# Kernel tuning notes

Hardware: AMD Instinct MI355X
Metric: run time of the kernel (lower is better)

Reference implementation:

```python
import jax, jax.numpy as jnp
import numpy as np
import math

EMB = 512

def setup_inputs() -> dict:
    key = jax.random.key(0)
    ks = jax.random.split(key, 7)
    B, L, E = 4, 4096, EMB
    s = 1.0 / math.sqrt(E)
    return {
        "x": jax.random.normal(ks[0], (B, L, E), dtype=jnp.float32),
        "Wq": jax.random.normal(ks[1], (E, E), dtype=jnp.float32) * s,
        "bq": jax.random.normal(ks[2], (E,), dtype=jnp.float32) * 0.01,
        "Wk": jax.random.normal(ks[3], (E, E), dtype=jnp.float32) * s,
        "bk": jax.random.normal(ks[4], (E,), dtype=jnp.float32) * 0.01,
        "Wv": jax.random.normal(ks[5], (E, E), dtype=jnp.float32) * s,
        "bv": jax.random.normal(ks[6], (E,), dtype=jnp.float32) * 0.01,
    }

def reference(x, Wq, bq, Wk, bk, Wv, bv):
    # x: [B, L, E]; Linear weights stored torch-style [out, in]
    E = x.shape[-1]
    L = x.shape[1]
    q = jnp.einsum('ble,fe->blf', x, Wq) + bq
    k = jnp.einsum('ble,fe->blf', x, Wk) + bk
    v = jnp.einsum('ble,fe->blf', x, Wv) + bv
    qk = jnp.einsum('bqe,bke->bqk', q, k)  # [B, L, L]
    # causal mask: strict upper triangle filled with -1e9 BEFORE scaling (as in source)
    mask = jnp.triu(jnp.ones((L, L), dtype=bool), k=1)
    qk = jnp.where(mask, jnp.float32(-1e9), qk)
    att = jax.nn.softmax(qk / jnp.sqrt(jnp.float32(E)), axis=-1)
    return jnp.einsum('bqk,bke->bqe', att, v)
```

## Files before the change

kernel.cpp:

```cpp
#include <hip/hip_runtime.h>

typedef unsigned short u16;
typedef unsigned int u32;
typedef short bf16x8 __attribute__((ext_vector_type(8)));
typedef float f32x4 __attribute__((ext_vector_type(4)));
typedef u16 u16x8 __attribute__((ext_vector_type(8)));
typedef u16 u16x4 __attribute__((ext_vector_type(4)));

typedef const __attribute__((address_space(1))) u32* gas_ptr;
typedef __attribute__((address_space(3))) u32* las_ptr;

#define LQ   4096
#define EMB  512
#define NB   4
#define MROWS (NB * LQ)
#define QSCALE 0.04419417382415922f

__device__ __forceinline__ u16 f2bf(float f) {
  unsigned u = __builtin_bit_cast(unsigned, f);
  u += 0x7fffu + ((u >> 16) & 1u);
  return (u16)(u >> 16);
}
__device__ __forceinline__ float bf2f(u16 h) {
  unsigned u = ((unsigned)h) << 16;
  return __builtin_bit_cast(float, u);
}

__global__ void prep_w(const float* __restrict__ Wq, const float* __restrict__ bq,
                       const float* __restrict__ Wk, const float* __restrict__ bk,
                       const float* __restrict__ Wv, const float* __restrict__ bv,
                       u16* __restrict__ wqb, u16* __restrict__ wkb, u16* __restrict__ wvb,
                       float* __restrict__ bias) {
  int i = blockIdx.x * 256 + threadIdx.x;
  if (i < EMB * EMB) {
    wqb[i] = f2bf(Wq[i] * QSCALE);
    wkb[i] = f2bf(Wk[i]);
    wvb[i] = f2bf(Wv[i]);
  }
  if (i < EMB) {
    bias[i]           = bq[i] * QSCALE;
    bias[EMB + i]     = bk[i];
    bias[2 * EMB + i] = bv[i];
  }
}

__global__ void prep_x(const float* __restrict__ x, u16* __restrict__ xb) {
  int i = blockIdx.x * 256 + threadIdx.x;
  const float4* p = (const float4*)(x + (size_t)i * 8);
  float4 a = p[0], b = p[1];
  u16x8 o;
  o[0] = f2bf(a.x); o[1] = f2bf(a.y); o[2] = f2bf(a.z); o[3] = f2bf(a.w);
  o[4] = f2bf(b.x); o[5] = f2bf(b.y); o[6] = f2bf(b.z); o[7] = f2bf(b.w);
  *(u16x8*)(xb + (size_t)i * 8) = o;
}

__device__ __forceinline__ void stage128_256t(const u16* g, int ld, u16* lds, int tid) {
  int wave = tid >> 6;
#pragma unroll
  for (int p = 0; p < 4; ++p) {
    int c = tid + p * 256;
    int row = c >> 3, hh = c & 7;
    int h = hh ^ (row & 7);
    const u16* src = g + (size_t)row * ld + h * 8;
    u16* dst = lds + wave * 512 + p * 2048;
    __builtin_amdgcn_global_load_lds((gas_ptr)(const void*)src, (las_ptr)(void*)dst, 16, 0, 0);
  }
}

__device__ __forceinline__ void gemm_core_db(
    const u16* __restrict__ A, int lda,
    const u16* __restrict__ B, int ldb,
    int kIters, u16* lds,
    f32x4 acc[4][4], int tid, int lane, int wr, int wc)
{
  stage128_256t(A, lda, lds, tid);
  stage128_256t(B, ldb, lds + 8192, tid);
  for (int kb = 0; kb < kIters; ++kb) {
    u16* ldsA = lds + (kb & 1) * 16384;
    u16* ldsB = ldsA + 8192;
    __syncthreads();
    if (kb + 1 < kIters) {
      u16* nA = lds + ((kb + 1) & 1) * 16384;
      stage128_256t(A + (kb + 1) * 64, lda, nA, tid);
      stage128_256t(B + (kb + 1) * 64, ldb, nA + 8192, tid);
    }
#pragma unroll
    for (int s = 0; s < 2; ++s) {
      bf16x8 af[4], bfr[4];
#pragma unroll
      for (int m = 0; m < 4; ++m) {
        int row = wr * 64 + m * 16 + (lane & 15);
        int hh = (s * 4 + (lane >> 4)) ^ (row & 7);
        af[m] = *(const bf16x8*)(ldsA + row * 64 + hh * 8);
      }
#pragma unroll
      for (int n = 0; n < 4; ++n) {
        int row = wc * 64 + n * 16 + (lane & 15);
        int hh = (s * 4 + (lane >> 4)) ^ (row & 7);
        bfr[n] = *(const bf16x8*)(ldsB + row * 64 + hh * 8);
      }
#pragma unroll
      for (int m = 0; m < 4; ++m)
#pragma unroll
        for (int n = 0; n < 4; ++n)
          acc[m][n] = __builtin_amdgcn_mfma_f32_16x16x32_bf16(af[m], bfr[n], acc[m][n], 0, 0, 0);
    }
  }
}

__global__ __launch_bounds__(256, 2) void k_qkv(
    const u16* __restrict__ xb,
    const u16* __restrict__ w0, const u16* __restrict__ w1, const u16* __restrict__ w2,
    const float* __restrict__ bias,
    u16* __restrict__ o0, u16* __restrict__ o1, u16* __restrict__ o2)
{
  __shared__ __align__(16) u16 lds[32768];
  int bi = blockIdx.x;
  int which = bi >> 9;
  int t = bi & 511;
  int rt = t >> 2, ct = t & 3;
  const u16* W = (which == 0) ? w0 : (which == 1) ? w1 : w2;
  const float* bs = bias + which * EMB;
  int tid = threadIdx.x, lane = tid & 63, wave = tid >> 6;
  int wr = wave >> 1, wc = wave & 1;
  f32x4 acc[4][4];
#pragma unroll
  for (int m = 0; m < 4; ++m)
#pragma unroll
    for (int n = 0; n < 4; ++n) acc[m][n] = (f32x4)0.0f;

  gemm_core_db(xb + (size_t)rt * 128 * EMB, EMB,
               W + (size_t)ct * 128 * EMB, EMB, EMB / 64,
               lds, acc, tid, lane, wr, wc);

#pragma unroll
  for (int m = 0; m < 4; ++m)
#pragma unroll
    for (int n = 0; n < 4; ++n) {
      int row0 = rt * 128 + wr * 64 + m * 16 + ((lane >> 4) << 2);
      int col  = ct * 128 + wc * 64 + n * 16 + (lane & 15);
      float bv = bs[col];
      if (which < 2) {
        u16* out = (which == 0) ? o0 : o1;
#pragma unroll
        for (int r = 0; r < 4; ++r)
          out[(size_t)(row0 + r) * EMB + col] = f2bf(acc[m][n][r] + bv);
      } else {
        int b = row0 >> 12, l0 = row0 & (LQ - 1);
        u16x4 pk;
#pragma unroll
        for (int r = 0; r < 4; ++r) pk[r] = f2bf(acc[m][n][r] + bv);
        *(u16x4*)(o2 + ((size_t)(b * EMB + col)) * LQ + l0) = pk;
      }
    }
}

__global__ __launch_bounds__(256, 2) void k_qk(
    const u16* __restrict__ Q, const u16* __restrict__ K,
    u16* __restrict__ S, int bstart)
{
  __shared__ __align__(16) u16 lds[32768];
  int t = blockIdx.x;
  int b_local = t / 528;
  int i = t - b_local * 528;
  int qi = (int)((sqrtf(8.f * (float)i + 1.f) - 1.f) * 0.5f);
  while ((qi + 1) * (qi + 2) / 2 <= i) ++qi;
  while (qi * (qi + 1) / 2 > i) --qi;
  int ki = i - qi * (qi + 1) / 2;
  int bg = bstart + b_local;

  int tid = threadIdx.x, lane = tid & 63, wave = tid >> 6;
  int wr = wave >> 1, wc = wave & 1;
  f32x4 acc[4][4];
#pragma unroll
  for (int m = 0; m < 4; ++m)
#pragma unroll
    for (int n = 0; n < 4; ++n) acc[m][n] = (f32x4)0.0f;

  gemm_core_db(Q + ((size_t)bg * LQ + qi * 128) * EMB, EMB,
               K + ((size_t)bg * LQ + ki * 128) * EMB, EMB, EMB / 64,
               lds, acc, tid, lane, wr, wc);

  u16* Sb = S + (size_t)b_local * LQ * LQ;
#pragma unroll
  for (int m = 0; m < 4; ++m)
#pragma unroll
    for (int n = 0; n < 4; ++n) {
      int row0 = qi * 128 + wr * 64 + m * 16 + ((lane >> 4) << 2);
      int col  = ki * 128 + wc * 64 + n * 16 + (lane & 15);
#pragma unroll
      for (int r = 0; r < 4; ++r) {
        int row = row0 + r;
        float v = (col > row) ? -1e9f : acc[m][n][r];
        Sb[(size_t)row * LQ + col] = f2bf(v);
      }
    }
}

__global__ __launch_bounds__(1024, 4) void k_pv3(
    const u16* __restrict__ S, const u16* __restrict__ Vt,
    float* __restrict__ out, int bstart, int bcount)
{
  __shared__ __align__(16) u16 sV[32768];
  __shared__ __align__(16) u16 sP[8192];
  __shared__ float sF[128];
  __shared__ float sL[128];
  __shared__ int   sFlag[16];

  int bi = blockIdx.x;
  int per = 2 * bcount;
  int rt = bi / per;
  int rem = bi - rt * per;
  int ct = rem / bcount;
  int b_local = rem - ct * bcount;
  int bg = bstart + b_local;
  int units = 2 * (rt + 1);

  const u16* Sbase = S + ((size_t)b_local * LQ + rt * 128) * LQ;
  const u16* Vb = Vt + ((size_t)bg * EMB + ct * 256) * LQ;

  int tid = threadIdx.x, lane = tid & 63, wave = tid >> 6;
  int l15 = lane & 15, lhi = lane >> 4;
  int wr = wave >> 3, wn = wave & 7;
  int r0 = tid >> 3;
  int cc = tid & 7;

  f32x4 acc[4][2];
#pragma unroll
  for (int m = 0; m < 4; ++m)
#pragma unroll
    for (int n = 0; n < 2; ++n) acc[m][n] = (f32x4)0.0f;
  float mrun = -3.0e38f, lrun = 0.f;

  auto stageV = [&](int i, u16* buf) {
    const u16* gb = Vb + i * 64;
#pragma unroll
    for (int p = 0; p < 2; ++p) {
      int c = tid + p * 1024;
      int col = c >> 3, h = (c & 7) ^ (col & 7);
      __builtin_amdgcn_global_load_lds(
          (gas_ptr)(const void*)(gb + (size_t)col * LQ + h * 8),
          (las_ptr)(void*)(buf + wave * 512 + p * 8192), 16, 0, 0);
    }
  };

  auto softmax = [&](u16x8 ar, u16x8& pf, float& fo) {
    float sv[8];
#pragma unroll
    for (int j = 0; j < 8; ++j) sv[j] = bf2f(ar[j]);
    float mx = fmaxf(fmaxf(fmaxf(sv[0], sv[1]), fmaxf(sv[2], sv[3])),
                     fmaxf(fmaxf(sv[4], sv[5]), fmaxf(sv[6], sv[7])));
#pragma unroll
    for (int off = 1; off <= 4; off <<= 1) mx = fmaxf(mx, __shfl_xor(mx, off));
    float mn = (mx > mrun + 8.f) ? mx : mrun;
    float f = __expf(mrun - mn);
    mrun = mn;
    float t = 0.f;
#pragma unroll
    for (int j = 0; j < 8; ++j) {
      float e = __expf(sv[j] - mrun);
      t += e;
      pf[j] = f2bf(e);
    }
#pragma unroll
    for (int off = 1; off <= 4; off <<= 1) t += __shfl_xor(t, off);
    lrun = lrun * f + t;
    fo = f;
  };

  int hhP = (cc ^ (r0 & 7)) * 8;

  stageV(0, sV);
  {
    u16x8 ar = *(const u16x8*)(Sbase + (size_t)r0 * LQ + cc * 8);
    u16x8 pf; float f;
    softmax(ar, pf, f);
    *(u16x8*)(sP + r0 * 64 + hhP) = pf;
    if (cc == 0) sF[r0] = f;
    int fl = __any(f < 1.f) ? 1 : 0;
    if (lane == 0) sFlag[wave] = fl;
  }

  for (int i = 0; i < units; ++i) {
    u16* vb = sV + (i & 1) * 16384;
    __syncthreads();
    bool have = (i + 1 < units);
    if (have) stageV(i + 1, sV + ((i + 1) & 1) * 16384);
    u16x8 ar;
    if (have) ar = *(const u16x8*)(Sbase + (i + 1) * 64 + (size_t)r0 * LQ + cc * 8);

    int4 fA = *(const int4*)&sFlag[0];
    int4 fB = *(const int4*)&sFlag[4];
    int4 fC = *(const int4*)&sFlag[8];
    int4 fD = *(const int4*)&sFlag[12];
    if ((fA.x | fA.y | fA.z | fA.w) | (fB.x | fB.y | fB.z | fB.w) |
        (fC.x | fC.y | fC.z | fC.w) | (fD.x | fD.y | fD.z | fD.w)) {
#pragma unroll
      for (int m = 0; m < 4; ++m) {
        f32x4 sf = *(const f32x4*)&sF[wr * 64 + m * 16 + lhi * 4];
#pragma unroll
        for (int n = 0; n < 2; ++n)
#pragma unroll
          for (int r = 0; r < 4; ++r) acc[m][n][r] *= sf[r];
      }
    }

#pragma unroll
    for (int s = 0; s < 2; ++s) {
      bf16x8 bv[2];
#pragma unroll
      for (int n = 0; n < 2; ++n) {
        int col = wn * 32 + n * 16 + l15;
        bv[n] = *(const bf16x8*)(vb + col * 64 + ((s * 4 + lhi) ^ (col & 7)) * 8);
      }
#pragma unroll
      for (int m = 0; m < 4; ++m) {
        int row = wr * 64 + m * 16 + l15;
        bf16x8 pa = *(const bf16x8*)(sP + row * 64 + ((s * 4 + lhi) ^ (row & 7)) * 8);
#pragma unroll
        for (int n = 0; n < 2; ++n)
          acc[m][n] = __builtin_amdgcn_mfma_f32_16x16x32_bf16(pa, bv[n], acc[m][n], 0, 0, 0);
      }
    }

    u16x8 pf; float f = 1.f;
    if (have) softmax(ar, pf, f);

    __syncthreads();
    if (have) {
      *(u16x8*)(sP + r0 * 64 + hhP) = pf;
      if (cc == 0) sF[r0] = f;
      int fl = __any(f < 1.f) ? 1 : 0;
      if (lane == 0) sFlag[wave] = fl;
    }
  }

  if (cc == 0) sL[r0] = 1.0f / lrun;
  __syncthreads();
#pragma unroll
  for (int m = 0; m < 4; ++m) {
    f32x4 li = *(const f32x4*)&sL[wr * 64 + m * 16 + lhi * 4];
#pragma unroll
    for (int r = 0; r < 4; ++r) {
      int grow = rt * 128 + wr * 64 + m * 16 + lhi * 4 + r;
#pragma unroll
      for (int n = 0; n < 2; ++n) {
        int col = ct * 256 + wn * 32 + n * 16 + l15;
        out[((size_t)bg * LQ + grow) * EMB + col] = acc[m][n][r] * li[r];
      }
    }
  }
}

extern "C" void kernel_launch(void* const* d_in, const int* in_sizes, int n_in,
                              void* d_out, int out_size, void* d_ws, size_t ws_size,
                              hipStream_t stream) {
  const float* x  = (const float*)d_in[0];
  const float* Wq = (const float*)d_in[1];
  const float* bq = (const float*)d_in[2];
  const float* Wk = (const float*)d_in[3];
  const float* bk = (const float*)d_in[4];
  const float* Wv = (const float*)d_in[5];
  const float* bv = (const float*)d_in[6];

  char* ws = (char*)d_ws;
  size_t off = 0;
  u16* xb  = (u16*)(ws + off); off += (size_t)MROWS * EMB * 2;
  u16* wqb = (u16*)(ws + off); off += (size_t)EMB * EMB * 2;
  u16* wkb = (u16*)(ws + off); off += (size_t)EMB * EMB * 2;
  u16* wvb = (u16*)(ws + off); off += (size_t)EMB * EMB * 2;
  float* bias = (float*)(ws + off); off += 3 * EMB * 4;
  off = (off + 255) & ~(size_t)255;
  u16* Qb  = (u16*)(ws + off); off += (size_t)MROWS * EMB * 2;
  u16* Kb  = (u16*)(ws + off); off += (size_t)MROWS * EMB * 2;
  u16* Vtb = (u16*)(ws + off); off += (size_t)MROWS * EMB * 2;
  size_t fixed = off;
  size_t s_full = (size_t)NB * LQ * LQ * 2;
  int bcap = (ws_size >= fixed + s_full) ? NB : 1;
  u16* Sb = (u16*)(ws + fixed);

  prep_w<<<(EMB * EMB + 255) / 256, 256, 0, stream>>>(Wq, bq, Wk, bk, Wv, bv,
                                                      wqb, wkb, wvb, bias);
  prep_x<<<(MROWS * EMB / 8) / 256, 256, 0, stream>>>(x, xb);

  k_qkv<<<1536, 256, 0, stream>>>(xb, wqb, wkb, wvb, bias, Qb, Kb, Vtb);

  for (int bs = 0; bs < NB; bs += bcap) {
    int bc = (bs + bcap <= NB) ? bcap : (NB - bs);
    k_qk<<<528 * bc, 256, 0, stream>>>(Qb, Kb, Sb, bs);
    k_pv3<<<64 * bc, 1024, 0, stream>>>(Sb, Vtb, (float*)d_out, bs, bc);
  }
}
```

Measured before the change: 236.7 us.

## Triple-buffer V and double-buffer P in PV kernel, one barrier per step

The PV kernel moves from a double-buffered V tile to a triple-buffered one, prefetched two steps ahead, and double-buffers the P/scale/flag shared arrays. This lets each iteration use a single barrier with explicit vmcnt/lgkmcnt waits instead of two __syncthreads. The goal is to hide global load latency and cut barrier stalls. In exchange it raises LDS use to roughly 130 KB per block, and the hand-written waitcnt counts depend on how the stageV loads are issued.

```diff
diff --git a/kernel.cpp b/kernel.cpp
--- a/kernel.cpp
+++ b/kernel.cpp
@@ -201,11 +201,11 @@
     const u16* __restrict__ S, const u16* __restrict__ Vt,
     float* __restrict__ out, int bstart, int bcount)
 {
-  __shared__ __align__(16) u16 sV[32768];
-  __shared__ __align__(16) u16 sP[8192];
-  __shared__ float sF[128];
+  __shared__ __align__(16) u16 sV[49152];
+  __shared__ __align__(16) u16 sP[16384];
+  __shared__ float sF[256];
   __shared__ float sL[128];
-  __shared__ int   sFlag[16];
+  __shared__ int   sFlag[32];
 
   int bi = blockIdx.x;
   int per = 2 * bcount;
@@ -270,34 +270,48 @@
 
   int hhP = (cc ^ (r0 & 7)) * 8;
 
+  auto publish = [&](int buf, u16x8 pf, float f) {
+    *(u16x8*)(sP + buf * 8192 + r0 * 64 + hhP) = pf;
+    if (cc == 0) sF[buf * 128 + r0] = f;
+    int fl = __any(f < 1.f) ? 1 : 0;
+    if (lane == 0) sFlag[buf * 16 + wave] = fl;
+  };
+
   stageV(0, sV);
+  u16x8 ar = *(const u16x8*)(Sbase + (size_t)r0 * LQ + cc * 8);
+  stageV(1, sV + 16384);
+  asm volatile("s_waitcnt vmcnt(2)" ::: "memory");
+  __builtin_amdgcn_sched_barrier(0);
   {
-    u16x8 ar = *(const u16x8*)(Sbase + (size_t)r0 * LQ + cc * 8);
     u16x8 pf; float f;
     softmax(ar, pf, f);
-    *(u16x8*)(sP + r0 * 64 + hhP) = pf;
-    if (cc == 0) sF[r0] = f;
-    int fl = __any(f < 1.f) ? 1 : 0;
-    if (lane == 0) sFlag[wave] = fl;
-  }
-
+    publish(0, pf, f);
+  }
+  asm volatile("s_waitcnt lgkmcnt(0)" ::: "memory");
+  __builtin_amdgcn_s_barrier();
+
+  int vc = 0;
   for (int i = 0; i < units; ++i) {
-    u16* vb = sV + (i & 1) * 16384;
-    __syncthreads();
-    bool have = (i + 1 < units);
-    if (have) stageV(i + 1, sV + ((i + 1) & 1) * 16384);
-    u16x8 ar;
-    if (have) ar = *(const u16x8*)(Sbase + (i + 1) * 64 + (size_t)r0 * LQ + cc * 8);
-
-    int4 fA = *(const int4*)&sFlag[0];
-    int4 fB = *(const int4*)&sFlag[4];
-    int4 fC = *(const int4*)&sFlag[8];
-    int4 fD = *(const int4*)&sFlag[12];
-    if ((fA.x | fA.y | fA.z | fA.w) | (fB.x | fB.y | fB.z | fB.w) |
-        (fC.x | fC.y | fC.z | fC.w) | (fD.x | fD.y | fD.z | fD.w)) {
+    u16* vb = sV + vc * 16384;
+    u16* pb = sP + (i & 1) * 8192;
+    bool haveA = (i + 1 < units);
+    bool haveS = (i + 2 < units);
+
+    if (haveA) ar = *(const u16x8*)(Sbase + (i + 1) * 64 + (size_t)r0 * LQ + cc * 8);
+    if (haveS) {
+      int vs = vc + 2; if (vs >= 3) vs -= 3;
+      stageV(i + 2, sV + vs * 16384);
+    }
+    __builtin_amdgcn_sched_barrier(0);
+
+    int fb = (i & 1) * 16;
+    int anyf = 0;
+#pragma unroll
+    for (int q = 0; q < 16; ++q) anyf |= sFlag[fb + q];
+    if (anyf) {
 #pragma unroll
       for (int m = 0; m < 4; ++m) {
-        f32x4 sf = *(const f32x4*)&sF[wr * 64 + m * 16 + lhi * 4];
+        f32x4 sf = *(const f32x4*)&sF[(i & 1) * 128 + wr * 64 + m * 16 + lhi * 4];
 #pragma unroll
         for (int n = 0; n < 2; ++n)
 #pragma unroll
@@ -316,23 +330,26 @@
 #pragma unroll
       for (int m = 0; m < 4; ++m) {
         int row = wr * 64 + m * 16 + l15;
-        bf16x8 pa = *(const bf16x8*)(sP + row * 64 + ((s * 4 + lhi) ^ (row & 7)) * 8);
+        bf16x8 pa = *(const bf16x8*)(pb + row * 64 + ((s * 4 + lhi) ^ (row & 7)) * 8);
 #pragma unroll
         for (int n = 0; n < 2; ++n)
           acc[m][n] = __builtin_amdgcn_mfma_f32_16x16x32_bf16(pa, bv[n], acc[m][n], 0, 0, 0);
       }
     }
 
-    u16x8 pf; float f = 1.f;
-    if (have) softmax(ar, pf, f);
-
-    __syncthreads();
-    if (have) {
-      *(u16x8*)(sP + r0 * 64 + hhP) = pf;
-      if (cc == 0) sF[r0] = f;
-      int fl = __any(f < 1.f) ? 1 : 0;
-      if (lane == 0) sFlag[wave] = fl;
-    }
+    if (haveA) {
+      if (haveS) asm volatile("s_waitcnt vmcnt(2)" ::: "memory");
+      else       asm volatile("s_waitcnt vmcnt(0)" ::: "memory");
+      __builtin_amdgcn_sched_barrier(0);
+      u16x8 pf; float f;
+      softmax(ar, pf, f);
+      publish((i + 1) & 1, pf, f);
+    }
+    asm volatile("s_waitcnt lgkmcnt(0)" ::: "memory");
+    __builtin_amdgcn_sched_barrier(0);
+    __builtin_amdgcn_s_barrier();
+
+    vc = (vc + 1 == 3) ? 0 : vc + 1;
   }
 
   if (cc == 0) sL[r0] = 1.0f / lrun;
```

After: 228.9 us. -3.3%, faster.
